# Kernel optimization log

Measured on AMD Instinct MI355X. Metric: run time of the kernel, lower is better.

## Reference

```python
import jax, jax.numpy as jnp
from jax import lax
import numpy as np

N_FEATURES = 64
B, H, W = 2, 64, 64
EPS = 1e-12  # F.normalize default eps


def setup_inputs() -> dict:
    key = jax.random.key(0)
    ks = jax.random.split(key, 10)
    L = N_FEATURES
    s = 0.02
    return {
        "x": jax.random.normal(ks[0], (B, L, H, W), dtype=jnp.float32),
        "conv1_w": jax.random.normal(ks[1], (L, L, 3, 3), dtype=jnp.float32) * s,
        "conv1_b": jax.random.normal(ks[2], (L,), dtype=jnp.float32) * s,
        "conv2_w": jax.random.normal(ks[3], (L, L, 3, 3), dtype=jnp.float32) * s,
        "conv2_b": jax.random.normal(ks[4], (L,), dtype=jnp.float32) * s,
        "wq": jax.random.normal(ks[5], (L, L), dtype=jnp.float32) * s,
        "wk": jax.random.normal(ks[6], (L, L), dtype=jnp.float32) * s,
        "wv": jax.random.normal(ks[7], (L, L), dtype=jnp.float32) * s,
        "wo": jax.random.normal(ks[8], (L, L), dtype=jnp.float32) * s,
        "bo": jax.random.normal(ks[9], (L,), dtype=jnp.float32) * s,
    }


def _conv3x3(h, w, b):
    y = lax.conv_general_dilated(
        h, w, window_strides=(1, 1), padding=((1, 1), (1, 1)),
        dimension_numbers=("NCHW", "OIHW", "NCHW"))
    return y + b[None, :, None, None]


def _l2norm(a):
    return a / jnp.maximum(jnp.linalg.norm(a, axis=-1, keepdims=True), EPS)


def reference(x, conv1_w, conv1_b, conv2_w, conv2_b, wq, wk, wv, wo, bo):
    # embedding: conv3x3 -> relu -> conv3x3
    h = _conv3x3(x, conv1_w, conv1_b)
    h = jax.nn.relu(h)
    h = _conv3x3(h, conv2_w, conv2_b)  # [B, L, H, W]
    b, l, hh, ww = h.shape
    t = h.reshape(b, l, hh * ww).transpose(0, 2, 1)  # [B, HW, L]
    q = _l2norm(t @ wq.T)  # [B, HW, L]
    k = _l2norm(t @ wk.T)
    v = t @ wv.T
    # per-token rank-1 outer product scores: [B, HW, L, L]
    scores = q[..., :, None] * k[..., None, :]
    p = jax.nn.softmax(scores, axis=-1)
    out = jnp.einsum("bncd,bnd->bnc", p, v)  # [B, HW, L]
    out = out @ wo.T + bo
    out = out.transpose(0, 2, 1).reshape(b, l, hh, ww)
    return out + h
```

## Files before the change

kernel.cpp:

```cpp
#include <hip/hip_runtime.h>
#include <hip/hip_bf16.h>


#define IMG 262144

using frag_ab = __attribute__((ext_vector_type(8))) short;
using frag_cd = __attribute__((ext_vector_type(4))) float;
typedef unsigned u32x4 __attribute__((ext_vector_type(4)));
typedef float    f32x2 __attribute__((ext_vector_type(2)));
typedef float    f32x4 __attribute__((ext_vector_type(4)));

static __device__ inline unsigned short f2bf(float f) {
    unsigned u = __float_as_uint(f);
    return (unsigned short)((u + 0x7FFFu + ((u >> 16) & 1u)) >> 16);
}
static __device__ inline unsigned packbf(float a, float b) {
    return (unsigned)f2bf(a) | ((unsigned)f2bf(b) << 16);
}
static __device__ inline frag_ab pack8(f32x4 a, f32x4 b) {
    union { unsigned u[4]; frag_ab f; } r;
    r.u[0] = packbf(a[0], a[1]);
    r.u[1] = packbf(a[2], a[3]);
    r.u[2] = packbf(b[0], b[1]);
    r.u[3] = packbf(b[2], b[3]);
    return r.f;
}

#if __has_builtin(__builtin_amdgcn_exp2f)
#define EXP2F(x) __builtin_amdgcn_exp2f(x)
#else
#define EXP2F(x) __expf(0.6931471805599453f * (x))
#endif

__global__ __launch_bounds__(256) void prep_w(
    const float* __restrict__ w1, const float* __restrict__ w2,
    unsigned short* __restrict__ wt1, unsigned short* __restrict__ wt2)
{
    int i = blockIdx.x * 256 + threadIdx.x;
    int mat = i >= 36864;
    int j = i - mat * 36864;
    int tap = j >> 12;
    int oc  = (j >> 6) & 63;
    int ic  = j & 63;
    const float* w = mat ? w2 : w1;
    int g = oc >> 4, mm = oc & 15;
    int s = ic >> 5, qq = (ic >> 3) & 3, e = ic & 7;
    int dst = ((((tap * 4 + g) * 2 + s) * 4 + qq) * 16 + mm) * 8 + e;
    (mat ? wt2 : wt1)[dst] = f2bf(w[(oc * 64 + ic) * 9 + tap]);
}

__global__ __launch_bounds__(256, 2) void fused_k(
    const float* __restrict__ x,
    const unsigned short* __restrict__ wt1, const unsigned short* __restrict__ wt2,
    const float* __restrict__ b1, const float* __restrict__ b2,
    const float* __restrict__ wq, const float* __restrict__ wk,
    const float* __restrict__ wv, const float* __restrict__ wo,
    const float* __restrict__ bo, float* __restrict__ out)
{
    __shared__ __align__(16) unsigned short xt[5 * 20 * 72];
    __shared__ __align__(16) unsigned short r1[54 * 72];
    __shared__ __align__(16) float          t_lds[16 * 68];
    __shared__ __align__(16) unsigned       tp[16 * 36];
    __shared__ __align__(16) f32x2          kv[16 * 66];
    __shared__ __align__(16) unsigned       o_l32[16 * 36];
    __shared__ __align__(16) f32x2          nrm[4 * 17];

    const int tid  = threadIdx.x;
    const int b    = blockIdx.x >> 8;
    const int y    = (blockIdx.x >> 2) & 63;
    const int x0   = (blockIdx.x & 3) * 16;
    const int wv_  = tid >> 6;
    const int lane = tid & 63;
    const int m    = lane & 15;
    const int qd   = lane >> 4;
    const int oc0  = wv_ * 16;

    frag_ab A1[9][2];
    #pragma unroll
    for (int t = 0; t < 9; ++t)
        #pragma unroll
        for (int s = 0; s < 2; ++s)
            A1[t][s] = *(const frag_ab*)&wt1[(((t * 4 + wv_) * 2 + s) * 64 + lane) * 8];

    #pragma unroll
    for (int it = 0; it < 10; ++it) {
        int e    = it * 256 + tid;
        int grp  = e & 7;
        int pair = e >> 3;
        int row = pair >> 6, ic = pair & 63;
        int yy = y - 2 + row;
        int yc = min(max(yy, 0), 63);
        int gx0 = x0 - 8 + grp * 4;
        int gxl = min(max(gx0, 0), 60);
        f32x4 v = *(const f32x4*)&x[((b * 64 + ic) * 64 + yc) * 64 + gxl];
        #pragma unroll
        for (int j = 0; j < 4; ++j) {
            int gx  = gx0 + j;
            int xsl = gx - x0 + 2;
            if (xsl < 0 || xsl >= 20) continue;
            unsigned short val =
                (yy == yc && gx >= 0 && gx <= 63) ? f2bf(v[j]) : (unsigned short)0;
            xt[(row * 20 + xsl) * 72 + ic] = val;
        }
    }
    __syncthreads();

    int pb[4], rn_[4], xs_[4];
    bool nv[4];
    #pragma unroll
    for (int nt = 0; nt < 4; ++nt) {
        int n  = nt * 16 + m;
        int nc = min(n, 53);
        int rr = nc / 18, xx = nc - rr * 18;
        rn_[nt] = rr; xs_[nt] = xx; nv[nt] = (n < 54);
        pb[nt] = (rr * 20 + xx) * 72 + qd * 8;
    }
    frag_cd acc1[4];
    #pragma unroll
    for (int i = 0; i < 4; ++i) acc1[i] = (frag_cd){0.f, 0.f, 0.f, 0.f};

    #pragma unroll
    for (int ky = 0; ky < 3; ++ky)
        #pragma unroll
        for (int kx = 0; kx < 3; ++kx)
            #pragma unroll
            for (int s = 0; s < 2; ++s) {
                frag_ab a = A1[ky * 3 + kx][s];
                int off = (ky * 20 + kx) * 72 + s * 32;
                #pragma unroll
                for (int nt = 0; nt < 4; ++nt)
                    acc1[nt] = __builtin_amdgcn_mfma_f32_16x16x32_bf16(
                        a, *(const frag_ab*)&xt[pb[nt] + off], acc1[nt], 0, 0, 0);
            }

    frag_ab A2[9][2];
    #pragma unroll
    for (int t = 0; t < 9; ++t)
        #pragma unroll
        for (int s = 0; s < 2; ++s)
            A2[t][s] = *(const frag_ab*)&wt2[(((t * 4 + wv_) * 2 + s) * 64 + lane) * 8];

    frag_ab Aq[2], Ak[2], Av[2], Ao[2];
    #pragma unroll
    for (int s = 0; s < 2; ++s) {
        int rb = (oc0 + m) * 64 + s * 32 + qd * 8;
        Aq[s] = pack8(*(const f32x4*)&wq[rb], *(const f32x4*)&wq[rb + 4]);
        Ak[s] = pack8(*(const f32x4*)&wk[rb], *(const f32x4*)&wk[rb + 4]);
        Av[s] = pack8(*(const f32x4*)&wv[rb], *(const f32x4*)&wv[rb + 4]);
        Ao[s] = pack8(*(const f32x4*)&wo[rb], *(const f32x4*)&wo[rb + 4]);
    }

    {
        frag_cd b1f = *(const frag_cd*)&b1[oc0 + qd * 4];
        #pragma unroll
        for (int nt = 0; nt < 4; ++nt) {
            if (!nv[nt]) continue;
            int n = nt * 16 + m;
            int gy = y - 1 + rn_[nt];
            int gx = x0 - 1 + xs_[nt];
            bool oob = (gy < 0) | (gy > 63) | (gx < 0) | (gx > 63);
            #pragma unroll
            for (int r = 0; r < 4; ++r) {
                float v = fmaxf(acc1[nt][r] + b1f[r], 0.f);
                r1[n * 72 + oc0 + qd * 4 + r] = oob ? (unsigned short)0 : f2bf(v);
            }
        }
    }
    __syncthreads();

    frag_cd acc2 = (frag_cd){0.f, 0.f, 0.f, 0.f};
    #pragma unroll
    for (int ky = 0; ky < 3; ++ky)
        #pragma unroll
        for (int kx = 0; kx < 3; ++kx)
            #pragma unroll
            for (int s = 0; s < 2; ++s)
                acc2 = __builtin_amdgcn_mfma_f32_16x16x32_bf16(
                    A2[ky * 3 + kx][s],
                    *(const frag_ab*)&r1[(ky * 18 + m + kx) * 72 + s * 32 + qd * 8],
                    acc2, 0, 0, 0);

    {
        frag_cd b2f = *(const frag_cd*)&b2[oc0 + qd * 4];
        f32x4 hv;
        #pragma unroll
        for (int r = 0; r < 4; ++r) hv[r] = acc2[r] + b2f[r];
        *(f32x4*)&t_lds[m * 68 + oc0 + qd * 4] = hv;
        int dpb = m * 36 + (oc0 >> 1) + qd * 2;
        tp[dpb + 0] = packbf(hv[0], hv[1]);
        tp[dpb + 1] = packbf(hv[2], hv[3]);
    }
    __syncthreads();

    frag_cd qA = (frag_cd){0,0,0,0}, kA = (frag_cd){0,0,0,0}, vA = (frag_cd){0,0,0,0};
    #pragma unroll
    for (int s = 0; s < 2; ++s) {
        frag_ab hfrag = *(const frag_ab*)&tp[m * 36 + s * 16 + qd * 4];
        qA = __builtin_amdgcn_mfma_f32_16x16x32_bf16(Aq[s], hfrag, qA, 0, 0, 0);
        kA = __builtin_amdgcn_mfma_f32_16x16x32_bf16(Ak[s], hfrag, kA, 0, 0, 0);
        vA = __builtin_amdgcn_mfma_f32_16x16x32_bf16(Av[s], hfrag, vA, 0, 0, 0);
    }

    float nq = qA[0]*qA[0] + qA[1]*qA[1] + qA[2]*qA[2] + qA[3]*qA[3];
    float nk = kA[0]*kA[0] + kA[1]*kA[1] + kA[2]*kA[2] + kA[3]*kA[3];
    nq += __shfl_xor(nq, 16); nq += __shfl_xor(nq, 32);
    nk += __shfl_xor(nk, 16); nk += __shfl_xor(nk, 32);
    if (qd == 0) nrm[wv_ * 17 + m] = (f32x2){nq, nk};
    #pragma unroll
    for (int r = 0; r < 4; ++r)
        kv[m * 66 + oc0 + qd * 4 + r] = (f32x2){kA[r], vA[r]};
    __syncthreads();

    f32x2 p0 = nrm[m],      p1 = nrm[17 + m];
    f32x2 p2 = nrm[34 + m], p3 = nrm[51 + m];
    float snq = p0.x + p1.x + p2.x + p3.x;
    float snk = p0.y + p1.y + p2.y + p3.y;
    float qs = 1.4426950408889634f /
               (fmaxf(sqrtf(snq), 1e-12f) * fmaxf(sqrtf(snk), 1e-12f));
    float qn[4];
    #pragma unroll
    for (int r = 0; r < 4; ++r) qn[r] = qA[r] * qs;

    float den[4] = {0, 0, 0, 0}, num[4] = {0, 0, 0, 0};
    #pragma unroll 8
    for (int d2 = 0; d2 < 32; ++d2) {
        f32x4 K = *(const f32x4*)&kv[m * 66 + d2 * 2];
        #pragma unroll
        for (int r = 0; r < 4; ++r) {
            float e0 = EXP2F(qn[r] * K[0]); den[r] += e0; num[r] = fmaf(e0, K[1], num[r]);
            float e1 = EXP2F(qn[r] * K[2]); den[r] += e1; num[r] = fmaf(e1, K[3], num[r]);
        }
    }
    {
        int ob = m * 36 + wv_ * 8 + qd * 2;
        o_l32[ob + 0] = packbf(num[0] / den[0], num[1] / den[1]);
        o_l32[ob + 1] = packbf(num[2] / den[2], num[3] / den[3]);
    }
    __syncthreads();

    frag_cd oA = (frag_cd){0, 0, 0, 0};
    #pragma unroll
    for (int s = 0; s < 2; ++s)
        oA = __builtin_amdgcn_mfma_f32_16x16x32_bf16(
            Ao[s], *(const frag_ab*)&o_l32[m * 36 + s * 16 + qd * 4], oA, 0, 0, 0);

    f32x4 bo4 = *(const f32x4*)&bo[oc0 + qd * 4];
    f32x4 res = *(const f32x4*)&t_lds[m * 68 + oc0 + qd * 4];
    #pragma unroll
    for (int r = 0; r < 4; ++r) {
        float v = oA[r] + bo4[r] + res[r];
        out[((b * 64 + oc0 + qd * 4 + r) * 64 + y) * 64 + x0 + m] = v;
    }
}

extern "C" void kernel_launch(void* const* d_in, const int* in_sizes, int n_in,
                              void* d_out, int out_size, void* d_ws, size_t ws_size,
                              hipStream_t stream) {
    const float* x  = (const float*)d_in[0];
    const float* w1 = (const float*)d_in[1];
    const float* b1 = (const float*)d_in[2];
    const float* w2 = (const float*)d_in[3];
    const float* b2 = (const float*)d_in[4];
    const float* wq = (const float*)d_in[5];
    const float* wk = (const float*)d_in[6];
    const float* wv = (const float*)d_in[7];
    const float* wo = (const float*)d_in[8];
    const float* bo = (const float*)d_in[9];
    float* out = (float*)d_out;

    unsigned short* wt1 = (unsigned short*)d_ws;
    unsigned short* wt2 = wt1 + 36864;

    prep_w<<<288, 256, 0, stream>>>(w1, w2, wt1, wt2);
    fused_k<<<512, 256, 0, stream>>>(x, wt1, wt2, b1, b2,
                                     wq, wk, wv, wo, bo, out);
}
```

Before: 91.21 us.

## Fuse weight prep into main kernel via per-block LDS transpose of conv weights

Removes the separate prep_w launch, so every block now loads the fp32 conv weights itself, converts them to bf16 into a shared staging buffer, and gathers its MFMA fragments from there. The x tile loads are issued into registers ahead of this work so their latency overlaps the weight staging. This drops one kernel launch and the workspace round trip. In exchange, each of the 512 blocks redundantly reads 2x147KB of weights, does strided 16-bit LDS gathers and extra barriers, and uses a larger 74KB shared buffer, which may reduce occupancy.

```diff
diff --git a/kernel.cpp b/kernel.cpp
--- a/kernel.cpp
+++ b/kernel.cpp
@@ -6,9 +6,8 @@
 
 using frag_ab = __attribute__((ext_vector_type(8))) short;
 using frag_cd = __attribute__((ext_vector_type(4))) float;
-typedef unsigned u32x4 __attribute__((ext_vector_type(4)));
-typedef float    f32x2 __attribute__((ext_vector_type(2)));
-typedef float    f32x4 __attribute__((ext_vector_type(4)));
+typedef float f32x2 __attribute__((ext_vector_type(2)));
+typedef float f32x4 __attribute__((ext_vector_type(4)));
 
 static __device__ inline unsigned short f2bf(float f) {
     unsigned u = __float_as_uint(f);
@@ -16,14 +15,6 @@
 }
 static __device__ inline unsigned packbf(float a, float b) {
     return (unsigned)f2bf(a) | ((unsigned)f2bf(b) << 16);
-}
-static __device__ inline frag_ab pack8(f32x4 a, f32x4 b) {
-    union { unsigned u[4]; frag_ab f; } r;
-    r.u[0] = packbf(a[0], a[1]);
-    r.u[1] = packbf(a[2], a[3]);
-    r.u[2] = packbf(b[0], b[1]);
-    r.u[3] = packbf(b[2], b[3]);
-    return r.f;
 }
 
 #if __has_builtin(__builtin_amdgcn_exp2f)
@@ -32,38 +23,24 @@
 #define EXP2F(x) __expf(0.6931471805599453f * (x))
 #endif
 
-__global__ __launch_bounds__(256) void prep_w(
-    const float* __restrict__ w1, const float* __restrict__ w2,
-    unsigned short* __restrict__ wt1, unsigned short* __restrict__ wt2)
-{
-    int i = blockIdx.x * 256 + threadIdx.x;
-    int mat = i >= 36864;
-    int j = i - mat * 36864;
-    int tap = j >> 12;
-    int oc  = (j >> 6) & 63;
-    int ic  = j & 63;
-    const float* w = mat ? w2 : w1;
-    int g = oc >> 4, mm = oc & 15;
-    int s = ic >> 5, qq = (ic >> 3) & 3, e = ic & 7;
-    int dst = ((((tap * 4 + g) * 2 + s) * 4 + qq) * 16 + mm) * 8 + e;
-    (mat ? wt2 : wt1)[dst] = f2bf(w[(oc * 64 + ic) * 9 + tap]);
-}
-
-__global__ __launch_bounds__(256, 2) void fused_k(
+__global__ __launch_bounds__(256, 2) void mega_k(
     const float* __restrict__ x,
-    const unsigned short* __restrict__ wt1, const unsigned short* __restrict__ wt2,
-    const float* __restrict__ b1, const float* __restrict__ b2,
+    const float* __restrict__ w1, const float* __restrict__ b1,
+    const float* __restrict__ w2, const float* __restrict__ b2,
     const float* __restrict__ wq, const float* __restrict__ wk,
     const float* __restrict__ wv, const float* __restrict__ wo,
     const float* __restrict__ bo, float* __restrict__ out)
 {
-    __shared__ __align__(16) unsigned short xt[5 * 20 * 72];
-    __shared__ __align__(16) unsigned short r1[54 * 72];
-    __shared__ __align__(16) float          t_lds[16 * 68];
-    __shared__ __align__(16) unsigned       tp[16 * 36];
-    __shared__ __align__(16) f32x2          kv[16 * 66];
-    __shared__ __align__(16) unsigned       o_l32[16 * 36];
-    __shared__ __align__(16) f32x2          nrm[4 * 17];
+    __shared__ __align__(16) unsigned char smem[74240];
+    unsigned short* cw    = (unsigned short*)smem;
+    unsigned short* aw    = (unsigned short*)smem;
+    unsigned short* xt    = (unsigned short*)smem;
+    unsigned short* r1    = (unsigned short*)(smem + 14400);
+    float*          t_lds = (float*)   (smem + 22176);
+    unsigned*       tp    = (unsigned*)(smem + 26528);
+    f32x2*          kv    = (f32x2*)   (smem + 28832);
+    unsigned*       o_l32 = (unsigned*)(smem + 37280);
+    f32x2*          nrm   = (f32x2*)   (smem + 39584);
 
     const int tid  = threadIdx.x;
     const int b    = blockIdx.x >> 8;
@@ -75,13 +52,7 @@
     const int qd   = lane >> 4;
     const int oc0  = wv_ * 16;
 
-    frag_ab A1[9][2];
-    #pragma unroll
-    for (int t = 0; t < 9; ++t)
-        #pragma unroll
-        for (int s = 0; s < 2; ++s)
-            A1[t][s] = *(const frag_ab*)&wt1[(((t * 4 + wv_) * 2 + s) * 64 + lane) * 8];
-
+    f32x4 xr[10];
     #pragma unroll
     for (int it = 0; it < 10; ++it) {
         int e    = it * 256 + tid;
@@ -92,7 +63,78 @@
         int yc = min(max(yy, 0), 63);
         int gx0 = x0 - 8 + grp * 4;
         int gxl = min(max(gx0, 0), 60);
-        f32x4 v = *(const f32x4*)&x[((b * 64 + ic) * 64 + yc) * 64 + gxl];
+        xr[it] = *(const f32x4*)&x[((b * 64 + ic) * 64 + yc) * 64 + gxl];
+    }
+
+    frag_ab A1[9][2], A2[9][2];
+    #pragma unroll
+    for (int mat = 0; mat < 2; ++mat) {
+        const float* wsrc = mat ? w2 : w1;
+        #pragma unroll
+        for (int it = 0; it < 36; ++it) {
+            int q4 = it * 256 + tid;
+            int row = q4 / 144;
+            int c4  = q4 - row * 144;
+            f32x4 v = *(const f32x4*)&wsrc[row * 576 + c4 * 4];
+            unsigned* dst = (unsigned*)&cw[row * 580 + c4 * 4];
+            dst[0] = packbf(v[0], v[1]);
+            dst[1] = packbf(v[2], v[3]);
+        }
+        __syncthreads();
+        #pragma unroll
+        for (int t = 0; t < 9; ++t)
+            #pragma unroll
+            for (int s = 0; s < 2; ++s) {
+                int base = (oc0 + m) * 580 + (s * 32 + qd * 8) * 9 + t;
+                union { unsigned u[4]; frag_ab f; } fr;
+                #pragma unroll
+                for (int p = 0; p < 4; ++p) {
+                    unsigned e0 = cw[base + (2 * p) * 9];
+                    unsigned e1 = cw[base + (2 * p + 1) * 9];
+                    fr.u[p] = e0 | (e1 << 16);
+                }
+                if (mat == 0) A1[t][s] = fr.f; else A2[t][s] = fr.f;
+            }
+        __syncthreads();
+    }
+
+    frag_ab Aq[2], Ak[2], Av[2], Ao[2];
+    {
+        #pragma unroll
+        for (int it = 0; it < 16; ++it) {
+            int q4 = it * 256 + tid;
+            int mat = q4 >> 10;
+            int r   = q4 & 1023;
+            int row = r >> 4, c4 = r & 15;
+            const float* wsrc = (mat == 0) ? wq : (mat == 1) ? wk
+                              : (mat == 2) ? wv : wo;
+            f32x4 v = *(const f32x4*)&wsrc[row * 64 + c4 * 4];
+            unsigned* dst = (unsigned*)&aw[mat * 4608 + row * 72 + c4 * 4];
+            dst[0] = packbf(v[0], v[1]);
+            dst[1] = packbf(v[2], v[3]);
+        }
+        __syncthreads();
+        #pragma unroll
+        for (int s = 0; s < 2; ++s) {
+            int off = (oc0 + m) * 72 + s * 32 + qd * 8;
+            Aq[s] = *(const frag_ab*)&aw[off];
+            Ak[s] = *(const frag_ab*)&aw[4608 + off];
+            Av[s] = *(const frag_ab*)&aw[9216 + off];
+            Ao[s] = *(const frag_ab*)&aw[13824 + off];
+        }
+        __syncthreads();
+    }
+
+    #pragma unroll
+    for (int it = 0; it < 10; ++it) {
+        int e    = it * 256 + tid;
+        int grp  = e & 7;
+        int pair = e >> 3;
+        int row = pair >> 6, ic = pair & 63;
+        int yy = y - 2 + row;
+        int yc = min(max(yy, 0), 63);
+        int gx0 = x0 - 8 + grp * 4;
+        f32x4 v = xr[it];
         #pragma unroll
         for (int j = 0; j < 4; ++j) {
             int gx  = gx0 + j;
@@ -132,23 +174,6 @@
                     acc1[nt] = __builtin_amdgcn_mfma_f32_16x16x32_bf16(
                         a, *(const frag_ab*)&xt[pb[nt] + off], acc1[nt], 0, 0, 0);
             }
-
-    frag_ab A2[9][2];
-    #pragma unroll
-    for (int t = 0; t < 9; ++t)
-        #pragma unroll
-        for (int s = 0; s < 2; ++s)
-            A2[t][s] = *(const frag_ab*)&wt2[(((t * 4 + wv_) * 2 + s) * 64 + lane) * 8];
-
-    frag_ab Aq[2], Ak[2], Av[2], Ao[2];
-    #pragma unroll
-    for (int s = 0; s < 2; ++s) {
-        int rb = (oc0 + m) * 64 + s * 32 + qd * 8;
-        Aq[s] = pack8(*(const f32x4*)&wq[rb], *(const f32x4*)&wq[rb + 4]);
-        Ak[s] = pack8(*(const f32x4*)&wk[rb], *(const f32x4*)&wk[rb + 4]);
-        Av[s] = pack8(*(const f32x4*)&wv[rb], *(const f32x4*)&wv[rb + 4]);
-        Ao[s] = pack8(*(const f32x4*)&wo[rb], *(const f32x4*)&wo[rb + 4]);
-    }
 
     {
         frag_cd b1f = *(const frag_cd*)&b1[oc0 + qd * 4];
@@ -268,10 +293,6 @@
     const float* bo = (const float*)d_in[9];
     float* out = (float*)d_out;
 
-    unsigned short* wt1 = (unsigned short*)d_ws;
-    unsigned short* wt2 = wt1 + 36864;
-
-    prep_w<<<288, 256, 0, stream>>>(w1, w2, wt1, wt2);
-    fused_k<<<512, 256, 0, stream>>>(x, wt1, wt2, b1, b2,
-                                     wq, wk, wv, wo, bo, out);
-}
+    mega_k<<<512, 256, 0, stream>>>(x, w1, b1, w2, b2,
+                                    wq, wk, wv, wo, bo, out);
+}
```

Measured after the change: 93.17 us. +2.1%, slower.
